# Optimization experiments

Measured on AMD Instinct MI355X. Metric: run time of the kernel, lower is better.

## Reference

```python
import jax, jax.numpy as jnp
import numpy as np

N = 8192
IN_F = 512
OUT_F = 128
NEG_BIG = -9.0e15


def setup_inputs() -> dict:
    key = jax.random.key(0)
    k_x, k_adj, k_w, k_a1, k_a2 = jax.random.split(key, 5)
    X = jax.random.normal(k_x, (N, IN_F), dtype=jnp.float32)
    adj = jax.random.randint(k_adj, (N, N), 0, 2, dtype=jnp.int32)
    # xavier_uniform with gain=1.414
    gain = 1.414
    lim_w = gain * np.sqrt(6.0 / (IN_F + OUT_F))
    W = jax.random.uniform(k_w, (IN_F, OUT_F), minval=-lim_w, maxval=lim_w, dtype=jnp.float32)
    lim_a = gain * np.sqrt(6.0 / (OUT_F + 1))
    a_1 = jax.random.uniform(k_a1, (OUT_F, 1), minval=-lim_a, maxval=lim_a, dtype=jnp.float32)
    a_2 = jax.random.uniform(k_a2, (OUT_F, 1), minval=-lim_a, maxval=lim_a, dtype=jnp.float32)
    return {"X": X, "adj": adj, "W": W, "a_1": a_1, "a_2": a_2}


def reference(X, adj, W, a_1, a_2):
    h = X @ W                         # [N, out]
    Wh1 = h @ a_1                     # [N, 1]
    Wh2 = h @ a_2                     # [N, 1]
    alpha = Wh1 + Wh2.T               # [N, N] broadcast score sum
    s = jax.nn.sigmoid(alpha)
    masked = jnp.where(adj > 0, s, jnp.float32(NEG_BIG))
    attn = jax.nn.softmax(masked, axis=1)  # dropout p=0.0 -> identity
    return attn @ h                   # [N, out]
```

## Files before the change

kernel.cpp:

```cpp
#include <hip/hip_runtime.h>
#include <hip/hip_bf16.h>

#define N_NODES 8192
#define IN_F 512
#define OUT_F 128
#define LOG2E 1.4426950408889634f

typedef unsigned short u16;
typedef unsigned int u32;
typedef short s16x8 __attribute__((ext_vector_type(8)));
typedef float f32x4 __attribute__((ext_vector_type(4)));
typedef u32 u32x4 __attribute__((ext_vector_type(4)));

__device__ __forceinline__ u16 f2bf(float f) {
    union { float f; unsigned u; } x; x.f = f;
    unsigned r = x.u + 0x7FFFu + ((x.u >> 16) & 1u);
    return (u16)(r >> 16);
}

__device__ __forceinline__ u32 packbf2(float a, float b) {
    return ((u32)f2bf(b) << 16) | (u32)f2bf(a);
}

__device__ __forceinline__ float edge_p(float wh1, float w2, int keep) {
    float alpha = wh1 + w2;
    float e = exp2f(-LOG2E * alpha);
    float s = __builtin_amdgcn_rcpf(1.0f + e);
    float p = exp2f(LOG2E * s);
    return keep ? p : 0.0f;
}

__device__ __forceinline__ u32 pack_p(float p0, float p1, float& psum) {
    u32 u = packbf2(p0, p1);
    union { u32 u; float f; } lo, hi;
    lo.u = u << 16;
    hi.u = u & 0xFFFF0000u;
    psum += lo.f + hi.f;
    return u;
}

__global__ void repack_W(const float* __restrict__ W, u16* __restrict__ W_frag) {
    int tid = blockIdx.x * 256 + threadIdx.x;
    int j = tid & 7;
    int lane = (tid >> 3) & 63;
    int nt = (tid >> 9) & 7;
    int kt = tid >> 12;
    int k = kt * 32 + (lane >> 4) * 8 + j;
    int n = nt * 16 + (lane & 15);
    W_frag[tid] = f2bf(W[k * OUT_F + n]);
}

__global__ void compute_Wa(const float* __restrict__ W, const float* __restrict__ a1,
                           const float* __restrict__ a2,
                           float* __restrict__ Wa1, float* __restrict__ Wa2) {
    int k = blockIdx.x * 256 + threadIdx.x;
    if (k >= IN_F) return;
    float s1 = 0.f, s2 = 0.f;
    for (int n = 0; n < OUT_F; n++) {
        float w = W[k * OUT_F + n];
        s1 += w * a1[n];
        s2 += w * a2[n];
    }
    Wa1[k] = s1; Wa2[k] = s2;
}

__global__ __launch_bounds__(256)
void gemm_h(const float* __restrict__ X, const u16* __restrict__ W_frag,
            const float* __restrict__ Wa1, const float* __restrict__ Wa2,
            float* __restrict__ Wh1, float* __restrict__ Wh2,
            u16* __restrict__ h_frag) {
    int tid = threadIdx.x;
    int wave = tid >> 6;
    int lane = tid & 63;
    int quad = lane >> 4;
    int lid = lane & 15;
    int rbase = blockIdx.x * 16;
    const float* xrow = X + (size_t)(rbase + lid) * IN_F;
    const s16x8* Wf = (const s16x8*)W_frag;
    f32x4 acc0 = {}, acc1 = {};
    float p1 = 0.f, p2 = 0.f;
    int nt0 = wave * 2;

    for (int kt = 0; kt < 16; kt++) {
        float4 x0 = *(const float4*)(xrow + kt * 32 + quad * 8);
        float4 x1 = *(const float4*)(xrow + kt * 32 + quad * 8 + 4);
        u32x4 uv;
        uv.x = packbf2(x0.x, x0.y); uv.y = packbf2(x0.z, x0.w);
        uv.z = packbf2(x1.x, x1.y); uv.w = packbf2(x1.z, x1.w);
        s16x8 a = __builtin_bit_cast(s16x8, uv);
        if (wave == 0) {
            float4 wa = *(const float4*)(Wa1 + kt * 32 + quad * 8);
            float4 wb = *(const float4*)(Wa1 + kt * 32 + quad * 8 + 4);
            float4 wc = *(const float4*)(Wa2 + kt * 32 + quad * 8);
            float4 wd = *(const float4*)(Wa2 + kt * 32 + quad * 8 + 4);
            p1 += x0.x*wa.x + x0.y*wa.y + x0.z*wa.z + x0.w*wa.w
                + x1.x*wb.x + x1.y*wb.y + x1.z*wb.z + x1.w*wb.w;
            p2 += x0.x*wc.x + x0.y*wc.y + x0.z*wc.z + x0.w*wc.w
                + x1.x*wd.x + x1.y*wd.y + x1.z*wd.z + x1.w*wd.w;
        }
        s16x8 b0 = Wf[(kt * 8 + nt0) * 64 + lane];
        s16x8 b1 = Wf[(kt * 8 + nt0 + 1) * 64 + lane];
        acc0 = __builtin_amdgcn_mfma_f32_16x16x32_bf16(a, b0, acc0, 0, 0, 0);
        acc1 = __builtin_amdgcn_mfma_f32_16x16x32_bf16(a, b1, acc1, 0, 0, 0);
    }

    #pragma unroll
    for (int reg = 0; reg < 4; reg++) {
        int row = rbase + quad * 4 + reg;
        int ktile = row >> 5, kl = row & 31;
        int lane2 = (kl >> 3) * 16 + lid, j2 = kl & 7;
        h_frag[(size_t)((ktile * 8 + nt0) * 64 + lane2) * 8 + j2] = f2bf(acc0[reg]);
        h_frag[(size_t)((ktile * 8 + nt0 + 1) * 64 + lane2) * 8 + j2] = f2bf(acc1[reg]);
    }
    if (wave == 0) {
        p1 += __shfl_xor(p1, 16, 64); p1 += __shfl_xor(p1, 32, 64);
        p2 += __shfl_xor(p2, 16, 64); p2 += __shfl_xor(p2, 32, 64);
        if (lane < 16) { Wh1[rbase + lid] = p1; Wh2[rbase + lid] = p2; }
    }
}

__global__ __launch_bounds__(256)
void attn_kernel(const int* __restrict__ adj, const float* __restrict__ Wh1,
                 const float* __restrict__ Wh2, const u16* __restrict__ h_frag,
                 float* __restrict__ out_part, float* __restrict__ sum_part,
                 int kshift) {
    int tid = threadIdx.x;
    int wave = tid >> 6;
    int lane = tid & 63;
    int quad = lane >> 4;
    int lid = lane & 15;
    int rtile = blockIdx.x >> kshift;
    int kh = blockIdx.x & ((1 << kshift) - 1);
    int rbase = rtile * 128 + wave * 32;
    int r0 = rbase + lid, r1 = r0 + 16;

    float wh10 = Wh1[r0], wh11 = Wh1[r1];
    f32x4 acc0[8] = {}, acc1[8] = {};
    float ps0 = 0.f, ps1 = 0.f;
    const s16x8* Hf = (const s16x8*)h_frag;
    const int* adjrow0 = adj + (size_t)r0 * N_NODES;
    const int* adjrow1 = adj + (size_t)r1 * N_NODES;

    int KT_PER = 256 >> kshift;
    int kt0 = kh * KT_PER;
    for (int kt = kt0; kt < kt0 + KT_PER; kt++) {
        int k0 = kt * 32 + quad * 8;
        int4 aj0a = *(const int4*)(adjrow0 + k0);
        int4 aj0b = *(const int4*)(adjrow0 + k0 + 4);
        int4 aj1a = *(const int4*)(adjrow1 + k0);
        int4 aj1b = *(const int4*)(adjrow1 + k0 + 4);
        float4 w20 = *(const float4*)(Wh2 + k0);
        float4 w21 = *(const float4*)(Wh2 + k0 + 4);

        u32x4 uv0, uv1;
        uv0.x = pack_p(edge_p(wh10, w20.x, aj0a.x), edge_p(wh10, w20.y, aj0a.y), ps0);
        uv0.y = pack_p(edge_p(wh10, w20.z, aj0a.z), edge_p(wh10, w20.w, aj0a.w), ps0);
        uv0.z = pack_p(edge_p(wh10, w21.x, aj0b.x), edge_p(wh10, w21.y, aj0b.y), ps0);
        uv0.w = pack_p(edge_p(wh10, w21.z, aj0b.z), edge_p(wh10, w21.w, aj0b.w), ps0);
        uv1.x = pack_p(edge_p(wh11, w20.x, aj1a.x), edge_p(wh11, w20.y, aj1a.y), ps1);
        uv1.y = pack_p(edge_p(wh11, w20.z, aj1a.z), edge_p(wh11, w20.w, aj1a.w), ps1);
        uv1.z = pack_p(edge_p(wh11, w21.x, aj1b.x), edge_p(wh11, w21.y, aj1b.y), ps1);
        uv1.w = pack_p(edge_p(wh11, w21.z, aj1b.z), edge_p(wh11, w21.w, aj1b.w), ps1);
        s16x8 af0 = __builtin_bit_cast(s16x8, uv0);
        s16x8 af1 = __builtin_bit_cast(s16x8, uv1);

        #pragma unroll
        for (int nt = 0; nt < 8; nt++) {
            s16x8 b = Hf[(kt * 8 + nt) * 64 + lane];
            acc0[nt] = __builtin_amdgcn_mfma_f32_16x16x32_bf16(af0, b, acc0[nt], 0, 0, 0);
            acc1[nt] = __builtin_amdgcn_mfma_f32_16x16x32_bf16(af1, b, acc1[nt], 0, 0, 0);
        }
    }

    ps0 += __shfl_xor(ps0, 16, 64); ps0 += __shfl_xor(ps0, 32, 64);
    ps1 += __shfl_xor(ps1, 16, 64); ps1 += __shfl_xor(ps1, 32, 64);
    if (quad == 0) {
        sum_part[(size_t)kh * N_NODES + r0] = ps0;
        sum_part[(size_t)kh * N_NODES + r1] = ps1;
    }

    #pragma unroll
    for (int nt = 0; nt < 8; nt++) {
        #pragma unroll
        for (int reg = 0; reg < 4; reg++) {
            int row0 = rbase + quad * 4 + reg;
            int col = nt * 16 + lid;
            out_part[((size_t)kh * N_NODES + row0) * OUT_F + col] = acc0[nt][reg];
            out_part[((size_t)kh * N_NODES + row0 + 16) * OUT_F + col] = acc1[nt][reg];
        }
    }
}

__global__ void finalize(const float* __restrict__ out_part,
                         const float* __restrict__ sum_part,
                         float* __restrict__ out, int kp) {
    int gid = blockIdx.x * 256 + threadIdx.x;
    int i = gid >> 7;
    float s = 0.f, v = 0.f;
    for (int kh = 0; kh < kp; kh++) {
        s += sum_part[(size_t)kh * N_NODES + i];
        v += out_part[(size_t)kh * N_NODES * OUT_F + gid];
    }
    out[gid] = v / s;
}

extern "C" void kernel_launch(void* const* d_in, const int* in_sizes, int n_in,
                              void* d_out, int out_size, void* d_ws, size_t ws_size,
                              hipStream_t stream) {
    const float* X   = (const float*)d_in[0];
    const int*   adj = (const int*)d_in[1];
    const float* W   = (const float*)d_in[2];
    const float* a1  = (const float*)d_in[3];
    const float* a2  = (const float*)d_in[4];

    const size_t BASE = (size_t)4 << 20;
    int kshift = 3;
    for (; kshift > 0; kshift--) {
        size_t kp = (size_t)1 << kshift;
        size_t need = BASE + kp * ((size_t)N_NODES * OUT_F * 4 + (size_t)N_NODES * 4);
        if (need <= ws_size) break;
    }
    int kp = 1 << kshift;

    char* ws = (char*)d_ws;
    float* Wh1 = (float*)(ws);
    float* Wh2 = (float*)(ws + (32 << 10));
    float* Wa1 = (float*)(ws + (64 << 10));
    float* Wa2 = (float*)(ws + (66 << 10));
    u16* W_frag = (u16*)(ws + (128 << 10));
    u16* h_frag = (u16*)(ws + (256 << 10));
    float* out_part = (float*)(ws + BASE);
    float* sum_part = (float*)(ws + BASE + ((size_t)kp << 22));
    float* out = (float*)d_out;

    hipLaunchKernelGGL(repack_W, dim3(256), dim3(256), 0, stream, W, W_frag);
    hipLaunchKernelGGL(compute_Wa, dim3(2), dim3(256), 0, stream, W, a1, a2, Wa1, Wa2);
    hipLaunchKernelGGL(gemm_h, dim3(512), dim3(256), 0, stream,
                       X, W_frag, Wa1, Wa2, Wh1, Wh2, h_frag);
    hipLaunchKernelGGL(attn_kernel, dim3(64 << kshift), dim3(256), 0, stream,
                       adj, Wh1, Wh2, h_frag, out_part, sum_part, kshift);
    hipLaunchKernelGGL(finalize, dim3((N_NODES * OUT_F) / 256), dim3(256), 0, stream,
                       out_part, sum_part, out, kp);
}
```

Before: 439.9 us.

## Increase attention K-split, stream adj with nontemporal loads, restructure h GEMM

```diff
diff --git a/kernel.cpp b/kernel.cpp
--- a/kernel.cpp
+++ b/kernel.cpp
@@ -4,6 +4,9 @@
 #define N_NODES 8192
 #define IN_F 512
 #define OUT_F 128
+#define KSHIFT 4
+#define KP (1 << KSHIFT)
+#define KT_PER (256 >> KSHIFT)
 #define LOG2E 1.4426950408889634f
 
 typedef unsigned short u16;
@@ -11,6 +14,7 @@
 typedef short s16x8 __attribute__((ext_vector_type(8)));
 typedef float f32x4 __attribute__((ext_vector_type(4)));
 typedef u32 u32x4 __attribute__((ext_vector_type(4)));
+typedef int i32x4 __attribute__((ext_vector_type(4)));
 
 __device__ __forceinline__ u16 f2bf(float f) {
     union { float f; unsigned u; } x; x.f = f;
@@ -19,7 +23,9 @@
 }
 
 __device__ __forceinline__ u32 packbf2(float a, float b) {
-    return ((u32)f2bf(b) << 16) | (u32)f2bf(a);
+    __hip_bfloat162 h = __float22bfloat162_rn(make_float2(a, b));
+    u32 u; __builtin_memcpy(&u, &h, 4);
+    return u;
 }
 
 __device__ __forceinline__ float edge_p(float wh1, float w2, int keep) {
@@ -28,15 +34,6 @@
     float s = __builtin_amdgcn_rcpf(1.0f + e);
     float p = exp2f(LOG2E * s);
     return keep ? p : 0.0f;
-}
-
-__device__ __forceinline__ u32 pack_p(float p0, float p1, float& psum) {
-    u32 u = packbf2(p0, p1);
-    union { u32 u; float f; } lo, hi;
-    lo.u = u << 16;
-    hi.u = u & 0xFFFF0000u;
-    psum += lo.f + hi.f;
-    return u;
 }
 
 __global__ void repack_W(const float* __restrict__ W, u16* __restrict__ W_frag) {
@@ -56,6 +53,7 @@
     int k = blockIdx.x * 256 + threadIdx.x;
     if (k >= IN_F) return;
     float s1 = 0.f, s2 = 0.f;
+    #pragma unroll 8
     for (int n = 0; n < OUT_F; n++) {
         float w = W[k * OUT_F + n];
         s1 += w * a1[n];
@@ -74,34 +72,33 @@
     int lane = tid & 63;
     int quad = lane >> 4;
     int lid = lane & 15;
-    int rbase = blockIdx.x * 16;
+    int rbase = blockIdx.x * 64 + wave * 16;
     const float* xrow = X + (size_t)(rbase + lid) * IN_F;
     const s16x8* Wf = (const s16x8*)W_frag;
-    f32x4 acc0 = {}, acc1 = {};
+    f32x4 acc[8] = {};
     float p1 = 0.f, p2 = 0.f;
-    int nt0 = wave * 2;
 
     for (int kt = 0; kt < 16; kt++) {
-        float4 x0 = *(const float4*)(xrow + kt * 32 + quad * 8);
-        float4 x1 = *(const float4*)(xrow + kt * 32 + quad * 8 + 4);
+        int k0 = kt * 32 + quad * 8;
+        float4 x0 = *(const float4*)(xrow + k0);
+        float4 x1 = *(const float4*)(xrow + k0 + 4);
         u32x4 uv;
         uv.x = packbf2(x0.x, x0.y); uv.y = packbf2(x0.z, x0.w);
         uv.z = packbf2(x1.x, x1.y); uv.w = packbf2(x1.z, x1.w);
         s16x8 a = __builtin_bit_cast(s16x8, uv);
-        if (wave == 0) {
-            float4 wa = *(const float4*)(Wa1 + kt * 32 + quad * 8);
-            float4 wb = *(const float4*)(Wa1 + kt * 32 + quad * 8 + 4);
-            float4 wc = *(const float4*)(Wa2 + kt * 32 + quad * 8);
-            float4 wd = *(const float4*)(Wa2 + kt * 32 + quad * 8 + 4);
-            p1 += x0.x*wa.x + x0.y*wa.y + x0.z*wa.z + x0.w*wa.w
-                + x1.x*wb.x + x1.y*wb.y + x1.z*wb.z + x1.w*wb.w;
-            p2 += x0.x*wc.x + x0.y*wc.y + x0.z*wc.z + x0.w*wc.w
-                + x1.x*wd.x + x1.y*wd.y + x1.z*wd.z + x1.w*wd.w;
+        float4 wa = *(const float4*)(Wa1 + k0);
+        float4 wb = *(const float4*)(Wa1 + k0 + 4);
+        float4 wc = *(const float4*)(Wa2 + k0);
+        float4 wd = *(const float4*)(Wa2 + k0 + 4);
+        p1 += x0.x*wa.x + x0.y*wa.y + x0.z*wa.z + x0.w*wa.w
+            + x1.x*wb.x + x1.y*wb.y + x1.z*wb.z + x1.w*wb.w;
+        p2 += x0.x*wc.x + x0.y*wc.y + x0.z*wc.z + x0.w*wc.w
+            + x1.x*wd.x + x1.y*wd.y + x1.z*wd.z + x1.w*wd.w;
+        #pragma unroll
+        for (int nt = 0; nt < 8; nt++) {
+            s16x8 b = Wf[(kt * 8 + nt) * 64 + lane];
+            acc[nt] = __builtin_amdgcn_mfma_f32_16x16x32_bf16(a, b, acc[nt], 0, 0, 0);
         }
-        s16x8 b0 = Wf[(kt * 8 + nt0) * 64 + lane];
-        s16x8 b1 = Wf[(kt * 8 + nt0 + 1) * 64 + lane];
-        acc0 = __builtin_amdgcn_mfma_f32_16x16x32_bf16(a, b0, acc0, 0, 0, 0);
-        acc1 = __builtin_amdgcn_mfma_f32_16x16x32_bf16(a, b1, acc1, 0, 0, 0);
     }
 
     #pragma unroll
@@ -109,28 +106,26 @@
         int row = rbase + quad * 4 + reg;
         int ktile = row >> 5, kl = row & 31;
         int lane2 = (kl >> 3) * 16 + lid, j2 = kl & 7;
-        h_frag[(size_t)((ktile * 8 + nt0) * 64 + lane2) * 8 + j2] = f2bf(acc0[reg]);
-        h_frag[(size_t)((ktile * 8 + nt0 + 1) * 64 + lane2) * 8 + j2] = f2bf(acc1[reg]);
-    }
-    if (wave == 0) {
-        p1 += __shfl_xor(p1, 16, 64); p1 += __shfl_xor(p1, 32, 64);
-        p2 += __shfl_xor(p2, 16, 64); p2 += __shfl_xor(p2, 32, 64);
-        if (lane < 16) { Wh1[rbase + lid] = p1; Wh2[rbase + lid] = p2; }
-    }
+        #pragma unroll
+        for (int nt = 0; nt < 8; nt++)
+            h_frag[(size_t)((ktile * 8 + nt) * 64 + lane2) * 8 + j2] = f2bf(acc[nt][reg]);
+    }
+    p1 += __shfl_xor(p1, 16, 64); p1 += __shfl_xor(p1, 32, 64);
+    p2 += __shfl_xor(p2, 16, 64); p2 += __shfl_xor(p2, 32, 64);
+    if (lane < 16) { Wh1[rbase + lid] = p1; Wh2[rbase + lid] = p2; }
 }
 
 __global__ __launch_bounds__(256)
 void attn_kernel(const int* __restrict__ adj, const float* __restrict__ Wh1,
                  const float* __restrict__ Wh2, const u16* __restrict__ h_frag,
-                 float* __restrict__ out_part, float* __restrict__ sum_part,
-                 int kshift) {
+                 float* __restrict__ out_part, float* __restrict__ sum_part) {
     int tid = threadIdx.x;
     int wave = tid >> 6;
     int lane = tid & 63;
     int quad = lane >> 4;
     int lid = lane & 15;
-    int rtile = blockIdx.x >> kshift;
-    int kh = blockIdx.x & ((1 << kshift) - 1);
+    int rtile = blockIdx.x >> KSHIFT;
+    int kh = blockIdx.x & (KP - 1);
     int rbase = rtile * 128 + wave * 32;
     int r0 = rbase + lid, r1 = r0 + 16;
 
@@ -138,29 +133,39 @@
     f32x4 acc0[8] = {}, acc1[8] = {};
     float ps0 = 0.f, ps1 = 0.f;
     const s16x8* Hf = (const s16x8*)h_frag;
-    const int* adjrow0 = adj + (size_t)r0 * N_NODES;
-    const int* adjrow1 = adj + (size_t)r1 * N_NODES;
-
-    int KT_PER = 256 >> kshift;
-    int kt0 = kh * KT_PER;
+    const i32x4* adjrow0 = (const i32x4*)(adj + (size_t)r0 * N_NODES);
+    const i32x4* adjrow1 = (const i32x4*)(adj + (size_t)r1 * N_NODES);
+
+    const int kt0 = kh * KT_PER;
+    #pragma unroll 4
     for (int kt = kt0; kt < kt0 + KT_PER; kt++) {
         int k0 = kt * 32 + quad * 8;
-        int4 aj0a = *(const int4*)(adjrow0 + k0);
-        int4 aj0b = *(const int4*)(adjrow0 + k0 + 4);
-        int4 aj1a = *(const int4*)(adjrow1 + k0);
-        int4 aj1b = *(const int4*)(adjrow1 + k0 + 4);
+        int q4 = k0 >> 2;
+        i32x4 aj0a = __builtin_nontemporal_load(adjrow0 + q4);
+        i32x4 aj0b = __builtin_nontemporal_load(adjrow0 + q4 + 1);
+        i32x4 aj1a = __builtin_nontemporal_load(adjrow1 + q4);
+        i32x4 aj1b = __builtin_nontemporal_load(adjrow1 + q4 + 1);
         float4 w20 = *(const float4*)(Wh2 + k0);
         float4 w21 = *(const float4*)(Wh2 + k0 + 4);
 
-        u32x4 uv0, uv1;
-        uv0.x = pack_p(edge_p(wh10, w20.x, aj0a.x), edge_p(wh10, w20.y, aj0a.y), ps0);
-        uv0.y = pack_p(edge_p(wh10, w20.z, aj0a.z), edge_p(wh10, w20.w, aj0a.w), ps0);
-        uv0.z = pack_p(edge_p(wh10, w21.x, aj0b.x), edge_p(wh10, w21.y, aj0b.y), ps0);
-        uv0.w = pack_p(edge_p(wh10, w21.z, aj0b.z), edge_p(wh10, w21.w, aj0b.w), ps0);
-        uv1.x = pack_p(edge_p(wh11, w20.x, aj1a.x), edge_p(wh11, w20.y, aj1a.y), ps1);
-        uv1.y = pack_p(edge_p(wh11, w20.z, aj1a.z), edge_p(wh11, w20.w, aj1a.w), ps1);
-        uv1.z = pack_p(edge_p(wh11, w21.x, aj1b.x), edge_p(wh11, w21.y, aj1b.y), ps1);
-        uv1.w = pack_p(edge_p(wh11, w21.z, aj1b.z), edge_p(wh11, w21.w, aj1b.w), ps1);
+        float e0 = edge_p(wh10, w20.x, aj0a.x), e1 = edge_p(wh10, w20.y, aj0a.y);
+        float e2 = edge_p(wh10, w20.z, aj0a.z), e3 = edge_p(wh10, w20.w, aj0a.w);
+        float e4 = edge_p(wh10, w21.x, aj0b.x), e5 = edge_p(wh10, w21.y, aj0b.y);
+        float e6 = edge_p(wh10, w21.z, aj0b.z), e7 = edge_p(wh10, w21.w, aj0b.w);
+        ps0 += ((e0 + e1) + (e2 + e3)) + ((e4 + e5) + (e6 + e7));
+        u32x4 uv0;
+        uv0.x = packbf2(e0, e1); uv0.y = packbf2(e2, e3);
+        uv0.z = packbf2(e4, e5); uv0.w = packbf2(e6, e7);
+
+        float f0 = edge_p(wh11, w20.x, aj1a.x), f1 = edge_p(wh11, w20.y, aj1a.y);
+        float f2 = edge_p(wh11, w20.z, aj1a.z), f3 = edge_p(wh11, w20.w, aj1a.w);
+        float f4 = edge_p(wh11, w21.x, aj1b.x), f5 = edge_p(wh11, w21.y, aj1b.y);
+        float f6 = edge_p(wh11, w21.z, aj1b.z), f7 = edge_p(wh11, w21.w, aj1b.w);
+        ps1 += ((f0 + f1) + (f2 + f3)) + ((f4 + f5) + (f6 + f7));
+        u32x4 uv1;
+        uv1.x = packbf2(f0, f1); uv1.y = packbf2(f2, f3);
+        uv1.z = packbf2(f4, f5); uv1.w = packbf2(f6, f7);
+
         s16x8 af0 = __builtin_bit_cast(s16x8, uv0);
         s16x8 af1 = __builtin_bit_cast(s16x8, uv1);
 
@@ -193,11 +198,12 @@
 
 __global__ void finalize(const float* __restrict__ out_part,
                          const float* __restrict__ sum_part,
-                         float* __restrict__ out, int kp) {
+                         float* __restrict__ out) {
     int gid = blockIdx.x * 256 + threadIdx.x;
     int i = gid >> 7;
     float s = 0.f, v = 0.f;
-    for (int kh = 0; kh < kp; kh++) {
+    #pragma unroll
+    for (int kh = 0; kh < KP; kh++) {
         s += sum_part[(size_t)kh * N_NODES + i];
         v += out_part[(size_t)kh * N_NODES * OUT_F + gid];
     }
@@ -214,14 +220,6 @@
     const float* a2  = (const float*)d_in[4];
 
     const size_t BASE = (size_t)4 << 20;
-    int kshift = 3;
-    for (; kshift > 0; kshift--) {
-        size_t kp = (size_t)1 << kshift;
-        size_t need = BASE + kp * ((size_t)N_NODES * OUT_F * 4 + (size_t)N_NODES * 4);
-        if (need <= ws_size) break;
-    }
-    int kp = 1 << kshift;
-
     char* ws = (char*)d_ws;
     float* Wh1 = (float*)(ws);
     float* Wh2 = (float*)(ws + (32 << 10));
@@ -230,15 +228,15 @@
     u16* W_frag = (u16*)(ws + (128 << 10));
     u16* h_frag = (u16*)(ws + (256 << 10));
     float* out_part = (float*)(ws + BASE);
-    float* sum_part = (float*)(ws + BASE + ((size_t)kp << 22));
+    float* sum_part = (float*)(ws + BASE + ((size_t)KP << 22));
     float* out = (float*)d_out;
 
     hipLaunchKernelGGL(repack_W, dim3(256), dim3(256), 0, stream, W, W_frag);
     hipLaunchKernelGGL(compute_Wa, dim3(2), dim3(256), 0, stream, W, a1, a2, Wa1, Wa2);
-    hipLaunchKernelGGL(gemm_h, dim3(512), dim3(256), 0, stream,
+    hipLaunchKernelGGL(gemm_h, dim3(128), dim3(256), 0, stream,
                        X, W_frag, Wa1, Wa2, Wh1, Wh2, h_frag);
-    hipLaunchKernelGGL(attn_kernel, dim3(64 << kshift), dim3(256), 0, stream,
-                       adj, Wh1, Wh2, h_frag, out_part, sum_part, kshift);
+    hipLaunchKernelGGL(attn_kernel, dim3(64 << KSHIFT), dim3(256), 0, stream,
+                       adj, Wh1, Wh2, h_frag, out_part, sum_part);
     hipLaunchKernelGGL(finalize, dim3((N_NODES * OUT_F) / 256), dim3(256), 0, stream,
-                       out_part, sum_part, out, kp);
-}
+                       out_part, sum_part, out);
+}
```

Result: slower. 509.2 us (+15.8%).
